# Kernel optimization log

Hardware: AMD Instinct MI355X
Metric: run time of the kernel (lower is better)

Reference implementation:

```python
import jax, jax.numpy as jnp
import numpy as np
import math

B, T, M, C, H = 4, 1024, 256, 512, 8
HD = C // H
NEG = -1e30


def setup_inputs() -> dict:
    key = jax.random.key(0)
    ks = jax.random.split(key, 16)
    s = 1.0 / math.sqrt(C)
    inp = {
        'x': jax.random.normal(ks[0], (B, T, C), jnp.float32),
        'y': jax.random.normal(ks[1], (B, M, C), jnp.float32),
        'attn_x_mask': jnp.tril(jnp.ones((T, T), bool))[None, None],  # causal (1,1,T,T)
        'Wqkv_x': jax.random.normal(ks[2], (C, 3 * C), jnp.float32) * s,
        'bqkv_x': jnp.zeros((3 * C,), jnp.float32),
        'Wqkv_y': jax.random.normal(ks[3], (C, 3 * C), jnp.float32) * s,
        'bqkv_y': jnp.zeros((3 * C,), jnp.float32),
        'w4x': jax.random.normal(ks[4], (H, HD), jnp.float32) * math.sqrt(1.0 / C / 3),
        'w4y': jax.random.normal(ks[5], (H, HD), jnp.float32) * math.sqrt(1.0 / C / 3),
        'w4xy': jax.random.normal(ks[6], (H, HD), jnp.float32) * math.sqrt(1.0 / C / 3),
        'Wgs': jax.random.normal(ks[7], (C, C), jnp.float32) * s,
        'bgs': jnp.zeros((C,), jnp.float32),
        'Wgc': jax.random.normal(ks[8], (C, C), jnp.float32) * s,
        'bgc': jnp.zeros((C,), jnp.float32),
        'Wp': jax.random.normal(ks[9], (C, C), jnp.float32) * s,
        'bp': jnp.zeros((C,), jnp.float32),
    }
    return inp


def _heads(t):
    b, n, c = t.shape
    return t.reshape(b, n, H, HD).transpose(0, 2, 1, 3)  # (B,H,N,HD)


def reference(x, y, attn_x_mask, Wqkv_x, bqkv_x, Wqkv_y, bqkv_y,
              w4x, w4y, w4xy, Wgs, bgs, Wgc, bgc, Wp, bp):
    q_x, k_x, v_x = [_heads(t) for t in jnp.split(x @ Wqkv_x + bqkv_x, 3, axis=-1)]
    q_y, k_y, v_y = [_heads(t) for t in jnp.split(y @ Wqkv_y + bqkv_y, 3, axis=-1)]
    scale = 1.0 / math.sqrt(HD)

    # additive bias attention: catt1 (per query-x), catt2 (per key-y), catt3 (bilinear)
    catt1 = jnp.einsum('bhtd,hd->bht', q_x, w4x)[..., :, None]          # (B,H,T,1)
    catt2 = jnp.einsum('bhmd,hd->bhm', q_y, w4y)[:, :, None, :]          # (B,H,1,M)
    catt3 = jnp.einsum('bhtd,bhmd->bhtm', q_x * w4xy[None, :, None, :], k_y) * scale
    catt = catt1 + catt2 + catt3                                         # (B,H,T,M)

    catt_x2y = jax.nn.softmax(catt, axis=-1)
    catt_y2x = jax.nn.softmax(catt, axis=-2)

    cval_x2y = jnp.einsum('bhtm,bhmd->bhtd', catt_x2y, v_y)
    cval_x2y = cval_x2y.transpose(0, 2, 1, 3).reshape(B, T, C)

    # product-of-attentions: (T,M) @ (M,T) -> (T,T)
    chain = jnp.einsum('bhtm,bhsm->bhts', catt_x2y, catt_y2x) * (1.0 / math.sqrt(M))
    chain = jnp.where(attn_x_mask, chain, NEG)
    chain = jax.nn.softmax(chain, axis=-1)
    cval_y2x = jnp.einsum('bhts,bhsd->bhtd', chain, v_x)
    cval_y2x = cval_y2x.transpose(0, 2, 1, 3).reshape(B, T, C)

    cval = cval_x2y + cval_y2x + x

    # masked self-attention
    satt = jnp.einsum('bhtd,bhsd->bhts', q_x, k_x) * scale
    satt = jnp.where(attn_x_mask, satt, NEG)
    satt = jax.nn.softmax(satt, axis=-1)
    sval = jnp.einsum('bhts,bhsd->bhtd', satt, v_x).transpose(0, 2, 1, 3).reshape(B, T, C)

    sgate = jax.nn.sigmoid(sval @ Wgs + bgs)
    cgate = jax.nn.sigmoid(cval @ Wgc + bgc)
    out = (sgate * cval + cgate * sval) @ Wp + bp
    return out
```

## Files before the change

### kernel.cpp

```cpp
#include <hip/hip_runtime.h>
#include <hip/hip_bf16.h>

typedef __hip_bfloat16 bf16;
using f4 = __attribute__((ext_vector_type(4))) float;
using s8 = __attribute__((ext_vector_type(8))) short;
using s4 = __attribute__((ext_vector_type(4))) short;

__device__ __forceinline__ void storeOut(float* p, float v) { *p = v; }
__device__ __forceinline__ void storeOut(bf16* p, float v) { *p = __float2bfloat16(v); }
__device__ __forceinline__ short bfs(float x) { return __builtin_bit_cast(short, __float2bfloat16(x)); }

constexpr int B_ = 4, T_ = 1024, M_ = 256, C_ = 512, H_ = 8, HD_ = 64, C3_ = 1536;

#define MFMA16(a, b, c) __builtin_amdgcn_mfma_f32_16x16x32_bf16((a), (b), (c), 0, 0, 0)

__global__ __launch_bounds__(256) void prep_kernel(
    const float* __restrict__ Wqkv_x, const float* __restrict__ Wqkv_y,
    const float* __restrict__ Wgs, const float* __restrict__ Wgc, const float* __restrict__ Wp,
    const float* __restrict__ x, const float* __restrict__ y,
    bf16* __restrict__ WT_x, bf16* __restrict__ WT_y, bf16* __restrict__ WT_gs,
    bf16* __restrict__ WT_gc, bf16* __restrict__ WT_p,
    bf16* __restrict__ x_bf, bf16* __restrict__ y_bf)
{
    __shared__ float Ls[64][65];
    const int tid = threadIdx.x;
    const int bid = blockIdx.x;
    if (bid < 576) {
        const float* W; bf16* WT; int N, t;
        if (bid < 192)      { W = Wqkv_x; WT = WT_x;  N = C3_; t = bid; }
        else if (bid < 384) { W = Wqkv_y; WT = WT_y;  N = C3_; t = bid - 192; }
        else if (bid < 448) { W = Wgs;    WT = WT_gs; N = C_;  t = bid - 384; }
        else if (bid < 512) { W = Wgc;    WT = WT_gc; N = C_;  t = bid - 448; }
        else                { W = Wp;     WT = WT_p;  N = C_;  t = bid - 512; }
        const int K = C_;
        const int tw = N >> 6;
        const int n0 = (t % tw) * 64, k0 = (t / tw) * 64;
        for (int i = tid; i < 1024; i += 256) {
            int kr = i >> 4, ng = i & 15;
            float4 v = *(const float4*)&W[(size_t)(k0 + kr) * N + n0 + ng * 4];
            Ls[ng * 4 + 0][kr] = v.x; Ls[ng * 4 + 1][kr] = v.y;
            Ls[ng * 4 + 2][kr] = v.z; Ls[ng * 4 + 3][kr] = v.w;
        }
        __syncthreads();
        for (int i = tid; i < 512; i += 256) {
            int n = i >> 3, kg = i & 7;
            s8 r;
            #pragma unroll
            for (int j = 0; j < 8; ++j) r[j] = bfs(Ls[n][kg * 8 + j]);
            *(s8*)&WT[(size_t)(n0 + n) * K + k0 + kg * 8] = r;
        }
    } else if (bid < 1600) {
        int i = (bid - 576) * 2048 + tid * 8;
        s8 r;
        #pragma unroll
        for (int j = 0; j < 8; ++j) r[j] = bfs(x[i + j]);
        *(s8*)&x_bf[i] = r;
    } else {
        int i = (bid - 1600) * 2048 + tid * 8;
        s8 r;
        #pragma unroll
        for (int j = 0; j < 8; ++j) r[j] = bfs(y[i + j]);
        *(s8*)&y_bf[i] = r;
    }
}

__global__ __launch_bounds__(256) void qwcatt_kernel(
    const bf16* __restrict__ qkv_x, const bf16* __restrict__ qkv_y,
    const float* __restrict__ w4x, const float* __restrict__ w4y,
    const float* __restrict__ w4xy,
    float* __restrict__ catt1b, float* __restrict__ catt2b, bf16* __restrict__ qw)
{
    const int bid = blockIdx.x;
    const int tid = threadIdx.x;
    if (bid < 160) {
        int i = bid * 256 + tid;
        const bf16* row; const float* w; float* out; int oi;
        if (i < 32768) {
            int bh = i >> 10, t = i & 1023, b = bh >> 3, h = bh & 7;
            row = qkv_x + (size_t)(b * T_ + t) * C3_ + h * HD_;
            w = w4x + h * HD_; out = catt1b; oi = i;
        } else {
            int j = i - 32768;
            int bh = j >> 8, m = j & 255, b = bh >> 3, h = bh & 7;
            row = qkv_y + (size_t)(b * M_ + m) * C3_ + h * HD_;
            w = w4y + h * HD_; out = catt2b; oi = j;
        }
        float s = 0.f;
        #pragma unroll
        for (int d = 0; d < HD_; ++d) s = fmaf(__bfloat162float(row[d]), w[d], s);
        out[oi] = s;
    } else {
        int o = ((bid - 160) * 256 + tid) * 8;
        int row = o >> 9, c = o & 511;
        const bf16* src = qkv_x + (size_t)row * C3_ + c;
        s8 r;
        #pragma unroll
        for (int j = 0; j < 8; ++j) r[j] = bfs(__bfloat162float(src[j]) * w4xy[c + j]);
        *(s8*)&qw[o] = r;
    }
}

template <typename OT>
__global__ __launch_bounds__(256) void gemm_staged_kernel(
    const bf16* __restrict__ A, const bf16* __restrict__ WT, const float* __restrict__ bias,
    OT* __restrict__ Cmat, int N, int K)
{
    __shared__ short Asb[128][72];
    __shared__ short Bsb[64][72];
    const int tid = threadIdx.x;
    const int wave = tid >> 6, lane = tid & 63;
    const int quad = lane >> 4, l16 = lane & 15;
    const int n0 = blockIdx.y * 64, m0 = blockIdx.x * 128;
    f4 acc[2][4];
    #pragma unroll
    for (int mt = 0; mt < 2; ++mt)
        #pragma unroll
        for (int nt = 0; nt < 4; ++nt) acc[mt][nt] = (f4)0.f;

    for (int k0 = 0; k0 < K; k0 += 64) {
        #pragma unroll
        for (int tl = 0; tl < 4; ++tl) {
            int g = tid + tl * 256, row = g >> 3, grp = g & 7;
            *(s8*)&Asb[row][grp * 8] = *(const s8*)&A[(size_t)(m0 + row) * K + k0 + grp * 8];
        }
        #pragma unroll
        for (int tl = 0; tl < 2; ++tl) {
            int g = tid + tl * 256, n = g >> 3, grp = g & 7;
            *(s8*)&Bsb[n][grp * 8] = *(const s8*)&WT[(size_t)(n0 + n) * K + k0 + grp * 8];
        }
        __syncthreads();
        #pragma unroll
        for (int ks = 0; ks < 2; ++ks) {
            s8 a0 = *(const s8*)&Asb[wave * 32 + l16][ks * 32 + quad * 8];
            s8 a1 = *(const s8*)&Asb[wave * 32 + 16 + l16][ks * 32 + quad * 8];
            #pragma unroll
            for (int nt = 0; nt < 4; ++nt) {
                s8 bv = *(const s8*)&Bsb[nt * 16 + l16][ks * 32 + quad * 8];
                acc[0][nt] = MFMA16(a0, bv, acc[0][nt]);
                acc[1][nt] = MFMA16(a1, bv, acc[1][nt]);
            }
        }
        __syncthreads();
    }
    #pragma unroll
    for (int mt = 0; mt < 2; ++mt)
        #pragma unroll
        for (int nt = 0; nt < 4; ++nt) {
            int col = n0 + nt * 16 + l16;
            float bb = bias[col];
            #pragma unroll
            for (int reg = 0; reg < 4; ++reg) {
                int row = m0 + wave * 32 + mt * 16 + quad * 4 + reg;
                storeOut(&Cmat[(size_t)row * N + col], acc[mt][nt][reg] + bb);
            }
        }
}

__global__ __launch_bounds__(256) void catt3r_kernel(
    const bf16* __restrict__ qw, const bf16* __restrict__ qkv_y,
    const float* __restrict__ catt1, const float* __restrict__ catt2,
    bf16* __restrict__ x2y, float* __restrict__ rowsum_, float* __restrict__ psum)
{
    __shared__ float redc[4][256];
    const int tid = threadIdx.x;
    const int wave = tid >> 6, lane = tid & 63;
    const int quad = lane >> 4, l16 = lane & 15;
    const int bh = blockIdx.x, b = bh >> 3, h = bh & 7;
    const int t0 = blockIdx.y * 64;
    f4 sc[4][4];
    #pragma unroll
    for (int mt = 0; mt < 4; ++mt)
        #pragma unroll
        for (int nt = 0; nt < 4; ++nt) sc[mt][nt] = (f4)0.f;

    const bf16* ap = qw + (size_t)(b * T_ + t0 + wave * 16 + l16) * C_ + h * HD_ + quad * 8;
    s8 a0 = *(const s8*)ap;
    s8 a1 = *(const s8*)(ap + 32);
    const bf16* bp = qkv_y + (size_t)(b * M_ + l16) * C3_ + C_ + h * HD_ + quad * 8;
    #pragma unroll
    for (int mt = 0; mt < 4; ++mt)
        #pragma unroll
        for (int nt = 0; nt < 4; ++nt) {
            const bf16* bq = bp + (size_t)(mt * 64 + nt * 16) * C3_;
            sc[mt][nt] = MFMA16(a0, *(const s8*)bq, sc[mt][nt]);
            sc[mt][nt] = MFMA16(a1, *(const s8*)(bq + 32), sc[mt][nt]);
        }

    float c1[4];
    #pragma unroll
    for (int reg = 0; reg < 4; ++reg)
        c1[reg] = catt1[bh * T_ + t0 + wave * 16 + quad * 4 + reg];
    #pragma unroll
    for (int mt = 0; mt < 4; ++mt)
        #pragma unroll
        for (int nt = 0; nt < 4; ++nt) {
            float c2 = catt2[bh * M_ + mt * 64 + nt * 16 + l16];
            #pragma unroll
            for (int reg = 0; reg < 4; ++reg)
                sc[mt][nt][reg] = __expf(sc[mt][nt][reg] * 0.125f + c1[reg] + c2);
        }

    #pragma unroll
    for (int reg = 0; reg < 4; ++reg) {
        float rs = 0.f;
        #pragma unroll
        for (int mt = 0; mt < 4; ++mt)
            #pragma unroll
            for (int nt = 0; nt < 4; ++nt) rs += sc[mt][nt][reg];
        rs += __shfl_xor(rs, 1); rs += __shfl_xor(rs, 2);
        rs += __shfl_xor(rs, 4); rs += __shfl_xor(rs, 8);
        const int t = t0 + wave * 16 + quad * 4 + reg;
        if (l16 == 0) rowsum_[bh * T_ + t] = rs;
        const float ri = 1.f / rs;
        #pragma unroll
        for (int mt = 0; mt < 4; ++mt)
            #pragma unroll
            for (int nt = 0; nt < 4; ++nt)
                x2y[((size_t)bh * T_ + t) * M_ + mt * 64 + nt * 16 + l16] =
                    __float2bfloat16(sc[mt][nt][reg] * ri);
    }

    #pragma unroll
    for (int mt = 0; mt < 4; ++mt)
        #pragma unroll
        for (int nt = 0; nt < 4; ++nt) {
            float es = sc[mt][nt][0] + sc[mt][nt][1] + sc[mt][nt][2] + sc[mt][nt][3];
            es += __shfl_xor(es, 16);
            es += __shfl_xor(es, 32);
            if (quad == 0) redc[wave][mt * 64 + nt * 16 + l16] = es;
        }
    __syncthreads();
    psum[((size_t)bh * 16 + blockIdx.y) * M_ + tid] =
        redc[0][tid] + redc[1][tid] + redc[2][tid] + redc[3][tid];
}

__global__ __launch_bounds__(256) void colfin_vtrans_kernel(
    const float* __restrict__ psum, float* __restrict__ colinv,
    const bf16* __restrict__ qkv_x, const bf16* __restrict__ qkv_y,
    bf16* __restrict__ vTx, bf16* __restrict__ vTy)
{
    __shared__ short Ls[64][68];
    const int tid = threadIdx.x;
    int bid = blockIdx.x;
    if (bid < 32) {
        const int bh = bid, m = tid;
        float s = 0.f;
        #pragma unroll
        for (int ch = 0; ch < 16; ++ch) s += psum[(bh * 16 + ch) * M_ + m];
        colinv[bh * M_ + m] = 1.f / s;
        return;
    }
    bid -= 32;
    const bf16* qkv; bf16* vT; int Nrows, bh, t0;
    if (bid < 512) { qkv = qkv_x; vT = vTx; Nrows = T_; bh = bid >> 4; t0 = (bid & 15) * 64; }
    else { bid -= 512; qkv = qkv_y; vT = vTy; Nrows = M_; bh = bid >> 2; t0 = (bid & 3) * 64; }
    const int b = bh >> 3, h = bh & 7;
    for (int i = tid; i < 4096; i += 256) {
        int tl = i >> 6, d = i & 63;
        Ls[d][tl] = __builtin_bit_cast(short,
            qkv[(size_t)(b * Nrows + t0 + tl) * C3_ + 2 * C_ + h * HD_ + d]);
    }
    __syncthreads();
    for (int i = tid; i < 4096; i += 256) {
        int d = i >> 6, tl = i & 63;
        vT[((size_t)bh * 64 + d) * Nrows + t0 + tl] = __builtin_bit_cast(bf16, Ls[d][tl]);
    }
}

__global__ __launch_bounds__(256) void y2xw_kernel(
    const bf16* __restrict__ x2y, const float* __restrict__ rowsum_,
    const float* __restrict__ colinv, bf16* __restrict__ y2x)
{
    const int i = (blockIdx.x * 256 + threadIdx.x) * 8;
    const int row = i >> 8, m = i & 255, bh = row >> 10;
    const float rs = rowsum_[row];
    s8 v = *(const s8*)&x2y[i];
    const float4 c0 = *(const float4*)&colinv[bh * M_ + m];
    const float4 c4 = *(const float4*)&colinv[bh * M_ + m + 4];
    float ci[8] = {c0.x, c0.y, c0.z, c0.w, c4.x, c4.y, c4.z, c4.w};
    s8 r;
    #pragma unroll
    for (int j = 0; j < 8; ++j)
        r[j] = bfs(__bfloat162float(__builtin_bit_cast(bf16, v[j])) * rs * ci[j]);
    *(s8*)&y2x[i] = r;
}

__global__ __launch_bounds__(256) void flash10_kernel(
    const bf16* __restrict__ x2y, const bf16* __restrict__ y2x,
    const bf16* __restrict__ vTx, const bf16* __restrict__ vTy,
    const bf16* __restrict__ qkv_x, const float* __restrict__ x,
    bf16* __restrict__ cval_bf, bf16* __restrict__ sval_bf)
{
    __shared__ short Kc[64][264];
    __shared__ short Ksf[64][72];
    __shared__ short Vb[64][72];
    __shared__ short Ps[4][16][68];
    const int tid = threadIdx.x;
    const int wave = tid >> 6, lane = tid & 63;
    const int quad = lane >> 4, l16 = lane & 15;
    const int bh = blockIdx.x, b = bh >> 3, h = bh & 7;
    const int jt = (blockIdx.y < 8) ? (15 - (int)blockIdx.y) : ((int)blockIdx.y - 8);
    const int rb = jt * 64 + wave * 16;
    const int nst = jt + 1;

    s8 qc[8], qs[2];
    {
        const bf16* qp = x2y + (size_t)(bh * T_ + rb + l16) * M_ + quad * 8;
        #pragma unroll
        for (int f = 0; f < 8; ++f) qc[f] = *(const s8*)(qp + f * 32);
        const bf16* qsp = qkv_x + (size_t)(b * T_ + rb + l16) * C3_ + h * HD_ + quad * 8;
        qs[0] = *(const s8*)qsp;
        qs[1] = *(const s8*)(qsp + 32);
    }

    f4 ocv[4];
    #pragma unroll
    for (int dt = 0; dt < 4; ++dt) ocv[dt] = (f4)0.f;
    {
        const bf16* vb = vTy + (size_t)(bh * 64 + l16) * M_ + quad * 8;
        #pragma unroll
        for (int f = 0; f < 8; ++f)
            #pragma unroll
            for (int dt = 0; dt < 4; ++dt) {
                s8 bv = *(const s8*)(vb + (size_t)dt * 16 * M_ + f * 32);
                ocv[dt] = MFMA16(qc[f], bv, ocv[dt]);
            }
    }

    f4 oc[4], os_[4];
    float lc[4] = {0.f, 0.f, 0.f, 0.f}, ls_[4] = {0.f, 0.f, 0.f, 0.f};
    #pragma unroll
    for (int dt = 0; dt < 4; ++dt) { oc[dt] = (f4)0.f; os_[dt] = (f4)0.f; }

    #pragma unroll
    for (int tl = 0; tl < 8; ++tl) {
        int g = tid + tl * 256, row = g >> 5, grp = g & 31;
        *(s8*)&Kc[row][grp * 8] = *(const s8*)&y2x[(size_t)(bh * T_ + row) * M_ + grp * 8];
    }
    #pragma unroll
    for (int tl = 0; tl < 2; ++tl) {
        int g = tid + tl * 256, row = g >> 3, grp = g & 7;
        *(s8*)&Ksf[row][grp * 8] =
            *(const s8*)&qkv_x[(size_t)(b * T_ + row) * C3_ + C_ + h * HD_ + grp * 8];
        *(s8*)&Vb[row][grp * 8] = *(const s8*)&vTx[(size_t)(bh * 64 + row) * T_ + grp * 8];
    }
    __syncthreads();

    for (int st = 0; st < nst; ++st) {
        const int s0 = st * 64;
        const bool pf = (st + 1) < nst;
        s8 kcp[8], ksp[2], vp[2];
        if (pf) {
            const int sn = s0 + 64;
            #pragma unroll
            for (int tl = 0; tl < 8; ++tl) {
                int g = tid + tl * 256, row = g >> 5, grp = g & 31;
                kcp[tl] = *(const s8*)&y2x[(size_t)(bh * T_ + sn + row) * M_ + grp * 8];
            }
            #pragma unroll
            for (int tl = 0; tl < 2; ++tl) {
                int g = tid + tl * 256, row = g >> 3, grp = g & 7;
                ksp[tl] = *(const s8*)&qkv_x[(size_t)(b * T_ + sn + row) * C3_ + C_ + h * HD_ + grp * 8];
                vp[tl] = *(const s8*)&vTx[(size_t)(bh * 64 + row) * T_ + sn + grp * 8];
            }
        }
        {
            f4 sc[4];
            #pragma unroll
            for (int nt = 0; nt < 4; ++nt) sc[nt] = (f4)0.f;
            #pragma unroll
            for (int f = 0; f < 8; ++f)
                #pragma unroll
                for (int nt = 0; nt < 4; ++nt) {
                    s8 bv = *(const s8*)&Kc[nt * 16 + l16][f * 32 + quad * 8];
                    sc[nt] = MFMA16(qc[f], bv, sc[nt]);
                }
            f4 ss[4];
            #pragma unroll
            for (int nt = 0; nt < 4; ++nt) ss[nt] = (f4)0.f;
            #pragma unroll
            for (int f = 0; f < 2; ++f)
                #pragma unroll
                for (int nt = 0; nt < 4; ++nt) {
                    s8 bv = *(const s8*)&Ksf[nt * 16 + l16][f * 32 + quad * 8];
                    ss[nt] = MFMA16(qs[f], bv, ss[nt]);
                }
            #pragma unroll
            for (int reg = 0; reg < 4; ++reg) {
                const int t_g = rb + quad * 4 + reg;
                #pragma unroll
                for (int nt = 0; nt < 4; ++nt) {
                    float pv = (s0 + nt * 16 + l16 <= t_g) ? __expf(sc[nt][reg] * (1.f / 16.f)) : 0.f;
                    lc[reg] += pv;
                    Ps[wave][quad * 4 + reg][nt * 16 + l16] = bfs(pv);
                }
            }
            #pragma unroll
            for (int ks = 0; ks < 2; ++ks) {
                const short* pp = &Ps[wave][l16][ks * 32 + quad * 8];
                s4 alo = *(const s4*)pp;
                s4 ahi = *(const s4*)(pp + 4);
                s8 a;
                a[0] = alo[0]; a[1] = alo[1]; a[2] = alo[2]; a[3] = alo[3];
                a[4] = ahi[0]; a[5] = ahi[1]; a[6] = ahi[2]; a[7] = ahi[3];
                #pragma unroll
                for (int dt = 0; dt < 4; ++dt) {
                    s8 bv = *(const s8*)&Vb[dt * 16 + l16][ks * 32 + quad * 8];
                    oc[dt] = MFMA16(a, bv, oc[dt]);
                }
            }
            #pragma unroll
            for (int reg = 0; reg < 4; ++reg) {
                const int t_g = rb + quad * 4 + reg;
                #pragma unroll
                for (int nt = 0; nt < 4; ++nt) {
                    float pv = (s0 + nt * 16 + l16 <= t_g) ? __expf(ss[nt][reg] * 0.125f) : 0.f;
                    ls_[reg] += pv;
                    Ps[wave][quad * 4 + reg][nt * 16 + l16] = bfs(pv);
                }
            }
            #pragma unroll
            for (int ks = 0; ks < 2; ++ks) {
                const short* pp = &Ps[wave][l16][ks * 32 + quad * 8];
                s4 alo = *(const s4*)pp;
                s4 ahi = *(const s4*)(pp + 4);
                s8 a;
                a[0] = alo[0]; a[1] = alo[1]; a[2] = alo[2]; a[3] = alo[3];
                a[4] = ahi[0]; a[5] = ahi[1]; a[6] = ahi[2]; a[7] = ahi[3];
                #pragma unroll
                for (int dt = 0; dt < 4; ++dt) {
                    s8 bv = *(const s8*)&Vb[dt * 16 + l16][ks * 32 + quad * 8];
                    os_[dt] = MFMA16(a, bv, os_[dt]);
                }
            }
        }
        __syncthreads();
        if (pf) {
            #pragma unroll
            for (int tl = 0; tl < 8; ++tl) {
                int g = tid + tl * 256, row = g >> 5, grp = g & 31;
                *(s8*)&Kc[row][grp * 8] = kcp[tl];
            }
            #pragma unroll
            for (int tl = 0; tl < 2; ++tl) {
                int g = tid + tl * 256, row = g >> 3, grp = g & 7;
                *(s8*)&Ksf[row][grp * 8] = ksp[tl];
                *(s8*)&Vb[row][grp * 8] = vp[tl];
            }
        }
        __syncthreads();
    }

    #pragma unroll
    for (int reg = 0; reg < 4; ++reg) {
        float l1 = lc[reg], l2 = ls_[reg];
        l1 += __shfl_xor(l1, 1); l1 += __shfl_xor(l1, 2);
        l1 += __shfl_xor(l1, 4); l1 += __shfl_xor(l1, 8);
        l2 += __shfl_xor(l2, 1); l2 += __shfl_xor(l2, 2);
        l2 += __shfl_xor(l2, 4); l2 += __shfl_xor(l2, 8);
        const float i1 = 1.f / l1, i2 = 1.f / l2;
        const int t = rb + quad * 4 + reg;
        #pragma unroll
        for (int dt = 0; dt < 4; ++dt) {
            size_t idx = (size_t)(b * T_ + t) * C_ + h * HD_ + dt * 16 + l16;
            float cv = ocv[dt][reg] + oc[dt][reg] * i1 + x[idx];
            cval_bf[idx] = __float2bfloat16(cv);
            float sv = os_[dt][reg] * i2;
            sval_bf[idx] = __float2bfloat16(sv);
        }
    }
}

__global__ __launch_bounds__(256) void gatefuse_kernel(
    const bf16* __restrict__ svalb, const bf16* __restrict__ cvalb,
    const bf16* __restrict__ WTgs, const bf16* __restrict__ WTgc,
    const float* __restrict__ bgs, const float* __restrict__ bgc,
    bf16* __restrict__ gated)
{
    __shared__ short Sb[128][72], Cb[128][72], W1b[64][72], W2b[64][72];
    const int tid = threadIdx.x;
    const int wave = tid >> 6, lane = tid & 63;
    const int quad = lane >> 4, l16 = lane & 15;
    const int n0 = blockIdx.y * 64, m0 = blockIdx.x * 128;
    f4 aS[2][4], aC[2][4];
    #pragma unroll
    for (int mt = 0; mt < 2; ++mt)
        #pragma unroll
        for (int nt = 0; nt < 4; ++nt) { aS[mt][nt] = (f4)0.f; aC[mt][nt] = (f4)0.f; }

    for (int k0 = 0; k0 < C_; k0 += 64) {
        #pragma unroll
        for (int tl = 0; tl < 4; ++tl) {
            int g = tid + tl * 256, row = g >> 3, grp = g & 7;
            *(s8*)&Sb[row][grp * 8] = *(const s8*)&svalb[(size_t)(m0 + row) * C_ + k0 + grp * 8];
            *(s8*)&Cb[row][grp * 8] = *(const s8*)&cvalb[(size_t)(m0 + row) * C_ + k0 + grp * 8];
        }
        #pragma unroll
        for (int tl = 0; tl < 2; ++tl) {
            int g = tid + tl * 256, n = g >> 3, grp = g & 7;
            *(s8*)&W1b[n][grp * 8] = *(const s8*)&WTgs[(size_t)(n0 + n) * C_ + k0 + grp * 8];
            *(s8*)&W2b[n][grp * 8] = *(const s8*)&WTgc[(size_t)(n0 + n) * C_ + k0 + grp * 8];
        }
        __syncthreads();
        #pragma unroll
        for (int ks = 0; ks < 2; ++ks) {
            s8 s0f = *(const s8*)&Sb[wave * 32 + l16][ks * 32 + quad * 8];
            s8 s1f = *(const s8*)&Sb[wave * 32 + 16 + l16][ks * 32 + quad * 8];
            s8 c0f = *(const s8*)&Cb[wave * 32 + l16][ks * 32 + quad * 8];
            s8 c1f = *(const s8*)&Cb[wave * 32 + 16 + l16][ks * 32 + quad * 8];
            #pragma unroll
            for (int nt = 0; nt < 4; ++nt) {
                s8 w1 = *(const s8*)&W1b[nt * 16 + l16][ks * 32 + quad * 8];
                s8 w2 = *(const s8*)&W2b[nt * 16 + l16][ks * 32 + quad * 8];
                aS[0][nt] = MFMA16(s0f, w1, aS[0][nt]);
                aS[1][nt] = MFMA16(s1f, w1, aS[1][nt]);
                aC[0][nt] = MFMA16(c0f, w2, aC[0][nt]);
                aC[1][nt] = MFMA16(c1f, w2, aC[1][nt]);
            }
        }
        __syncthreads();
    }
    #pragma unroll
    for (int mt = 0; mt < 2; ++mt)
        #pragma unroll
        for (int nt = 0; nt < 4; ++nt) {
            int col = n0 + nt * 16 + l16;
            float b1 = bgs[col], b2 = bgc[col];
            #pragma unroll
            for (int reg = 0; reg < 4; ++reg) {
                int row = m0 + wave * 32 + mt * 16 + quad * 4 + reg;
                size_t idx = (size_t)row * C_ + col;
                float gs = 1.f / (1.f + __expf(-(aS[mt][nt][reg] + b1)));
                float gc = 1.f / (1.f + __expf(-(aC[mt][nt][reg] + b2)));
                float cvv = __bfloat162float(cvalb[idx]);
                float svv = __bfloat162float(svalb[idx]);
                gated[idx] = __float2bfloat16(gs * cvv + gc * svv);
            }
        }
}

extern "C" void kernel_launch(void* const* d_in, const int* in_sizes, int n_in,
                              void* d_out, int out_size, void* d_ws, size_t ws_size,
                              hipStream_t stream)
{
    const float* x      = (const float*)d_in[0];
    const float* y      = (const float*)d_in[1];
    const float* Wqkv_x = (const float*)d_in[3];
    const float* bqkv_x = (const float*)d_in[4];
    const float* Wqkv_y = (const float*)d_in[5];
    const float* bqkv_y = (const float*)d_in[6];
    const float* w4x    = (const float*)d_in[7];
    const float* w4y    = (const float*)d_in[8];
    const float* w4xy   = (const float*)d_in[9];
    const float* Wgs    = (const float*)d_in[10];
    const float* bgs    = (const float*)d_in[11];
    const float* Wgc    = (const float*)d_in[12];
    const float* bgc    = (const float*)d_in[13];
    const float* Wp     = (const float*)d_in[14];
    const float* bp     = (const float*)d_in[15];

    float* ws = (float*)d_ws;
    bf16*  qkv_x_bf = (bf16*)(ws + 0);
    bf16*  qkv_y_bf = (bf16*)(ws + 3145728);
    bf16*  gated_bf = (bf16*)(ws + 3932160);
    bf16*  cval_bf  = (bf16*)(ws + 5242880);
    bf16*  x2y_bf   = (bf16*)(ws + 12320768);
    bf16*  x_bf     = x2y_bf;
    bf16*  y_bf     = (bf16*)(ws + 13369344);
    bf16*  y2x_bf   = (bf16*)(ws + 16515072);
    bf16*  vTx_bf   = (bf16*)(ws + 20709376);
    bf16*  vTy_bf   = (bf16*)(ws + 21757952);
    float* psum_    = ws + 22020096;
    bf16*  qw_bf    = (bf16*)(ws + 26214400);
    bf16*  sval_bf  = qw_bf;
    bf16*  WT_x     = (bf16*)(ws + 27262976);
    bf16*  WT_y     = (bf16*)(ws + 27656192);
    bf16*  WT_gs    = (bf16*)(ws + 28049408);
    bf16*  WT_gc    = (bf16*)(ws + 28180480);
    bf16*  WT_p    = (bf16*)(ws + 28311552);
    float* catt1b   = ws + 28442624;
    float* catt2b   = ws + 28475392;
    float* colinv   = ws + 28483584;
    float* rowsum_  = ws + 28491776;

    prep_kernel<<<1856, 256, 0, stream>>>(
        Wqkv_x, Wqkv_y, Wgs, Wgc, Wp, x, y,
        WT_x, WT_y, WT_gs, WT_gc, WT_p, x_bf, y_bf);

    gemm_staged_kernel<bf16><<<dim3(32, 24), 256, 0, stream>>>(x_bf, WT_x, bqkv_x, qkv_x_bf, C3_, C_);
    gemm_staged_kernel<bf16><<<dim3(8, 24), 256, 0, stream>>>(y_bf, WT_y, bqkv_y, qkv_y_bf, C3_, C_);

    qwcatt_kernel<<<1184, 256, 0, stream>>>(
        qkv_x_bf, qkv_y_bf, w4x, w4y, w4xy, catt1b, catt2b, qw_bf);

    catt3r_kernel<<<dim3(32, 16), 256, 0, stream>>>(
        qw_bf, qkv_y_bf, catt1b, catt2b, x2y_bf, rowsum_, psum_);

    colfin_vtrans_kernel<<<672, 256, 0, stream>>>(psum_, colinv, qkv_x_bf, qkv_y_bf, vTx_bf, vTy_bf);

    y2xw_kernel<<<4096, 256, 0, stream>>>(x2y_bf, rowsum_, colinv, y2x_bf);

    flash10_kernel<<<dim3(32, 16), 256, 0, stream>>>(
        x2y_bf, y2x_bf, vTx_bf, vTy_bf, qkv_x_bf, x, cval_bf, sval_bf);

    gatefuse_kernel<<<dim3(32, 8), 256, 0, stream>>>(
        sval_bf, cval_bf, WT_gs, WT_gc, bgs, bgc, gated_bf);

    gemm_staged_kernel<float><<<dim3(32, 8), 256, 0, stream>>>(
        gated_bf, WT_p, bp, (float*)d_out, C_, C_);
}
```

Baseline: 240.6 us.

## Pair short and long causal tiles per block with split-key wave groups

Replaces the flash attention kernel with a 512-thread version. Each block pairs a short causal query tile with its mirror long tile so every block runs nine balanced phases. One group of four waves handles the short tile fully and then the first part of the long tile. The other group handles the rest of the long tile, and the partial accumulators and row sums are merged through shared memory at the end. This removes the uneven per-block causal workload and tail imbalance, at the cost of doubled shared memory, an extra reduction and more synchronisation per phase.

Result: faster. 229.1 us (-4.8%).

```diff
diff --git a/kernel.cpp b/kernel.cpp
--- a/kernel.cpp
+++ b/kernel.cpp
@@ -285,30 +285,117 @@
     *(s8*)&y2x[i] = r;
 }
 
-__global__ __launch_bounds__(256) void flash10_kernel(
+__device__ __forceinline__ void attn_unit(
+    const short* __restrict__ Kc, const short* __restrict__ Ksf, const short* __restrict__ Vb,
+    short* __restrict__ PsW, const s8 qc[8], const s8 qs[2],
+    f4 (&oc)[4], f4 (&os)[4], float (&lc)[4], float (&ls)[4],
+    int s0, bool diag, int trow, int quad, int l16)
+{
+    f4 sc[4];
+    #pragma unroll
+    for (int nt = 0; nt < 4; ++nt) sc[nt] = (f4)0.f;
+    #pragma unroll
+    for (int f = 0; f < 8; ++f)
+        #pragma unroll
+        for (int nt = 0; nt < 4; ++nt) {
+            s8 bv = *(const s8*)&Kc[(nt * 16 + l16) * 264 + f * 32 + quad * 8];
+            sc[nt] = MFMA16(qc[f], bv, sc[nt]);
+        }
+    f4 ss[4];
+    #pragma unroll
+    for (int nt = 0; nt < 4; ++nt) ss[nt] = (f4)0.f;
+    #pragma unroll
+    for (int f = 0; f < 2; ++f)
+        #pragma unroll
+        for (int nt = 0; nt < 4; ++nt) {
+            s8 bv = *(const s8*)&Ksf[(nt * 16 + l16) * 72 + f * 32 + quad * 8];
+            ss[nt] = MFMA16(qs[f], bv, ss[nt]);
+        }
+    #pragma unroll
+    for (int reg = 0; reg < 4; ++reg) {
+        const int t_g = trow + quad * 4 + reg;
+        #pragma unroll
+        for (int nt = 0; nt < 4; ++nt) {
+            float pv = __expf(sc[nt][reg] * 0.0625f);
+            if (diag && (s0 + nt * 16 + l16 > t_g)) pv = 0.f;
+            lc[reg] += pv;
+            PsW[(quad * 4 + reg) * 68 + nt * 16 + l16] = bfs(pv);
+        }
+    }
+    #pragma unroll
+    for (int ks = 0; ks < 2; ++ks) {
+        const short* pp = &PsW[l16 * 68 + ks * 32 + quad * 8];
+        s4 alo = *(const s4*)pp;
+        s4 ahi = *(const s4*)(pp + 4);
+        s8 a;
+        a[0] = alo[0]; a[1] = alo[1]; a[2] = alo[2]; a[3] = alo[3];
+        a[4] = ahi[0]; a[5] = ahi[1]; a[6] = ahi[2]; a[7] = ahi[3];
+        #pragma unroll
+        for (int dt = 0; dt < 4; ++dt) {
+            s8 bv = *(const s8*)&Vb[(dt * 16 + l16) * 72 + ks * 32 + quad * 8];
+            oc[dt] = MFMA16(a, bv, oc[dt]);
+        }
+    }
+    #pragma unroll
+    for (int reg = 0; reg < 4; ++reg) {
+        const int t_g = trow + quad * 4 + reg;
+        #pragma unroll
+        for (int nt = 0; nt < 4; ++nt) {
+            float pv = __expf(ss[nt][reg] * 0.125f);
+            if (diag && (s0 + nt * 16 + l16 > t_g)) pv = 0.f;
+            ls[reg] += pv;
+            PsW[(quad * 4 + reg) * 68 + nt * 16 + l16] = bfs(pv);
+        }
+    }
+    #pragma unroll
+    for (int ks = 0; ks < 2; ++ks) {
+        const short* pp = &PsW[l16 * 68 + ks * 32 + quad * 8];
+        s4 alo = *(const s4*)pp;
+        s4 ahi = *(const s4*)(pp + 4);
+        s8 a;
+        a[0] = alo[0]; a[1] = alo[1]; a[2] = alo[2]; a[3] = alo[3];
+        a[4] = ahi[0]; a[5] = ahi[1]; a[6] = ahi[2]; a[7] = ahi[3];
+        #pragma unroll
+        for (int dt = 0; dt < 4; ++dt) {
+            s8 bv = *(const s8*)&Vb[(dt * 16 + l16) * 72 + ks * 32 + quad * 8];
+            os[dt] = MFMA16(a, bv, os[dt]);
+        }
+    }
+}
+
+__global__ __launch_bounds__(512, 2) void flash11_kernel(
     const bf16* __restrict__ x2y, const bf16* __restrict__ y2x,
     const bf16* __restrict__ vTx, const bf16* __restrict__ vTy,
     const bf16* __restrict__ qkv_x, const float* __restrict__ x,
     bf16* __restrict__ cval_bf, bf16* __restrict__ sval_bf)
 {
-    __shared__ short Kc[64][264];
-    __shared__ short Ksf[64][72];
-    __shared__ short Vb[64][72];
-    __shared__ short Ps[4][16][68];
+    __shared__ short KcA[64][264], KcB[64][264];
+    __shared__ short KsfA[64][72], KsfB[64][72];
+    __shared__ short VbA[64][72], VbB[64][72];
+    __shared__ short Ps[8][16][68];
     const int tid = threadIdx.x;
     const int wave = tid >> 6, lane = tid & 63;
     const int quad = lane >> 4, l16 = lane & 15;
     const int bh = blockIdx.x, b = bh >> 3, h = bh & 7;
-    const int jt = (blockIdx.y < 8) ? (15 - (int)blockIdx.y) : ((int)blockIdx.y - 8);
-    const int rb = jt * 64 + wave * 16;
-    const int nst = jt + 1;
+    const int p = blockIdx.y;
+    const int w = wave & 3;
+    const bool gA = wave < 4;
+    const int q2t = 15 - p;
+    const int rb1 = p * 64 + w * 16, rb2 = q2t * 64 + w * 16;
+    short* PsW = &Ps[wave][0][0];
+    const int tidg = tid & 255;
+
+    short (*Kc)[264] = gA ? KcA : KcB;
+    short (*Ksf)[72] = gA ? KsfA : KsfB;
+    short (*Vv)[72]  = gA ? VbA : VbB;
 
     s8 qc[8], qs[2];
     {
-        const bf16* qp = x2y + (size_t)(bh * T_ + rb + l16) * M_ + quad * 8;
+        const int rq = gA ? rb1 : rb2;
+        const bf16* qp = x2y + (size_t)(bh * T_ + rq + l16) * M_ + quad * 8;
         #pragma unroll
         for (int f = 0; f < 8; ++f) qc[f] = *(const s8*)(qp + f * 32);
-        const bf16* qsp = qkv_x + (size_t)(b * T_ + rb + l16) * C3_ + h * HD_ + quad * 8;
+        const bf16* qsp = qkv_x + (size_t)(b * T_ + rq + l16) * C3_ + h * HD_ + quad * 8;
         qs[0] = *(const s8*)qsp;
         qs[1] = *(const s8*)(qsp + 32);
     }
@@ -332,141 +419,151 @@
     #pragma unroll
     for (int dt = 0; dt < 4; ++dt) { oc[dt] = (f4)0.f; os_[dt] = (f4)0.f; }
 
-    #pragma unroll
-    for (int tl = 0; tl < 8; ++tl) {
-        int g = tid + tl * 256, row = g >> 5, grp = g & 31;
-        *(s8*)&Kc[row][grp * 8] = *(const s8*)&y2x[(size_t)(bh * T_ + row) * M_ + grp * 8];
-    }
-    #pragma unroll
-    for (int tl = 0; tl < 2; ++tl) {
-        int g = tid + tl * 256, row = g >> 3, grp = g & 7;
-        *(s8*)&Ksf[row][grp * 8] =
-            *(const s8*)&qkv_x[(size_t)(b * T_ + row) * C3_ + C_ + h * HD_ + grp * 8];
-        *(s8*)&Vb[row][grp * 8] = *(const s8*)&vTx[(size_t)(bh * 64 + row) * T_ + grp * 8];
+    {
+        const int s = gA ? 0 : (8 - p);
+        #pragma unroll
+        for (int tl = 0; tl < 8; ++tl) {
+            int g = tidg + tl * 256, row = g >> 5, grp = g & 31;
+            *(s8*)&Kc[row][grp * 8] = *(const s8*)&y2x[(size_t)(bh * T_ + s * 64 + row) * M_ + grp * 8];
+        }
+        #pragma unroll
+        for (int tl = 0; tl < 2; ++tl) {
+            int g = tidg + tl * 256, row = g >> 3, grp = g & 7;
+            *(s8*)&Ksf[row][grp * 8] =
+                *(const s8*)&qkv_x[(size_t)(b * T_ + s * 64 + row) * C3_ + C_ + h * HD_ + grp * 8];
+            *(s8*)&Vv[row][grp * 8] = *(const s8*)&vTx[(size_t)(bh * 64 + row) * T_ + s * 64 + grp * 8];
+        }
     }
     __syncthreads();
 
-    for (int st = 0; st < nst; ++st) {
-        const int s0 = st * 64;
-        const bool pf = (st + 1) < nst;
-        s8 kcp[8], ksp[2], vp[2];
-        if (pf) {
-            const int sn = s0 + 64;
+    for (int ph = 0; ph < 9; ++ph) {
+        int s, trow; bool active, diag;
+        if (gA) {
+            if (ph <= p) { s = ph;         diag = (ph == p); trow = rb1; }
+            else         { s = ph - p - 1; diag = false;     trow = rb2; }
+            active = true;
+        } else {
+            s = 8 - p + ph; diag = (ph == 7); trow = rb2;
+            active = (ph < 8);
+        }
+        int sn;
+        if (gA) sn = (ph < p) ? (ph + 1) : ((ph == p) ? 0 : ((ph < 8) ? (ph - p) : -1));
+        else    sn = (ph < 7) ? (s + 1) : -1;
+
+        s8 kc[8], ks[2], vb[2];
+        if (sn >= 0) {
             #pragma unroll
             for (int tl = 0; tl < 8; ++tl) {
-                int g = tid + tl * 256, row = g >> 5, grp = g & 31;
-                kcp[tl] = *(const s8*)&y2x[(size_t)(bh * T_ + sn + row) * M_ + grp * 8];
+                int g = tidg + tl * 256, row = g >> 5, grp = g & 31;
+                kc[tl] = *(const s8*)&y2x[(size_t)(bh * T_ + sn * 64 + row) * M_ + grp * 8];
             }
             #pragma unroll
             for (int tl = 0; tl < 2; ++tl) {
-                int g = tid + tl * 256, row = g >> 3, grp = g & 7;
-                ksp[tl] = *(const s8*)&qkv_x[(size_t)(b * T_ + sn + row) * C3_ + C_ + h * HD_ + grp * 8];
-                vp[tl] = *(const s8*)&vTx[(size_t)(bh * 64 + row) * T_ + sn + grp * 8];
-            }
-        }
-        {
-            f4 sc[4];
-            #pragma unroll
-            for (int nt = 0; nt < 4; ++nt) sc[nt] = (f4)0.f;
-            #pragma unroll
-            for (int f = 0; f < 8; ++f)
-                #pragma unroll
-                for (int nt = 0; nt < 4; ++nt) {
-                    s8 bv = *(const s8*)&Kc[nt * 16 + l16][f * 32 + quad * 8];
-                    sc[nt] = MFMA16(qc[f], bv, sc[nt]);
-                }
-            f4 ss[4];
-            #pragma unroll
-            for (int nt = 0; nt < 4; ++nt) ss[nt] = (f4)0.f;
-            #pragma unroll
-            for (int f = 0; f < 2; ++f)
-                #pragma unroll
-                for (int nt = 0; nt < 4; ++nt) {
-                    s8 bv = *(const s8*)&Ksf[nt * 16 + l16][f * 32 + quad * 8];
-                    ss[nt] = MFMA16(qs[f], bv, ss[nt]);
-                }
+                int g = tidg + tl * 256, row = g >> 3, grp = g & 7;
+                ks[tl] = *(const s8*)&qkv_x[(size_t)(b * T_ + sn * 64 + row) * C3_ + C_ + h * HD_ + grp * 8];
+                vb[tl] = *(const s8*)&vTx[(size_t)(bh * 64 + row) * T_ + sn * 64 + grp * 8];
+            }
+        }
+
+        if (active)
+            attn_unit(&Kc[0][0], &Ksf[0][0], &Vv[0][0], PsW, qc, qs,
+                      oc, os_, lc, ls_, s * 64, diag, trow, quad, l16);
+
+        if (gA && ph == p) {
             #pragma unroll
             for (int reg = 0; reg < 4; ++reg) {
-                const int t_g = rb + quad * 4 + reg;
-                #pragma unroll
-                for (int nt = 0; nt < 4; ++nt) {
-                    float pv = (s0 + nt * 16 + l16 <= t_g) ? __expf(sc[nt][reg] * (1.f / 16.f)) : 0.f;
-                    lc[reg] += pv;
-                    Ps[wave][quad * 4 + reg][nt * 16 + l16] = bfs(pv);
-                }
-            }
-            #pragma unroll
-            for (int ks = 0; ks < 2; ++ks) {
-                const short* pp = &Ps[wave][l16][ks * 32 + quad * 8];
-                s4 alo = *(const s4*)pp;
-                s4 ahi = *(const s4*)(pp + 4);
-                s8 a;
-                a[0] = alo[0]; a[1] = alo[1]; a[2] = alo[2]; a[3] = alo[3];
-                a[4] = ahi[0]; a[5] = ahi[1]; a[6] = ahi[2]; a[7] = ahi[3];
+                float l1 = lc[reg], l2 = ls_[reg];
+                l1 += __shfl_xor(l1, 1); l1 += __shfl_xor(l1, 2);
+                l1 += __shfl_xor(l1, 4); l1 += __shfl_xor(l1, 8);
+                l2 += __shfl_xor(l2, 1); l2 += __shfl_xor(l2, 2);
+                l2 += __shfl_xor(l2, 4); l2 += __shfl_xor(l2, 8);
+                const float i1 = 1.f / l1, i2 = 1.f / l2;
+                const int t = rb1 + quad * 4 + reg;
                 #pragma unroll
                 for (int dt = 0; dt < 4; ++dt) {
-                    s8 bv = *(const s8*)&Vb[dt * 16 + l16][ks * 32 + quad * 8];
-                    oc[dt] = MFMA16(a, bv, oc[dt]);
+                    size_t idx = (size_t)(b * T_ + t) * C_ + h * HD_ + dt * 16 + l16;
+                    cval_bf[idx] = __float2bfloat16(ocv[dt][reg] + oc[dt][reg] * i1 + x[idx]);
+                    sval_bf[idx] = __float2bfloat16(os_[dt][reg] * i2);
                 }
             }
+            const bf16* qp = x2y + (size_t)(bh * T_ + rb2 + l16) * M_ + quad * 8;
+            #pragma unroll
+            for (int f = 0; f < 8; ++f) qc[f] = *(const s8*)(qp + f * 32);
+            const bf16* qsp = qkv_x + (size_t)(b * T_ + rb2 + l16) * C3_ + h * HD_ + quad * 8;
+            qs[0] = *(const s8*)qsp;
+            qs[1] = *(const s8*)(qsp + 32);
+            #pragma unroll
+            for (int dt = 0; dt < 4; ++dt) { oc[dt] = (f4)0.f; os_[dt] = (f4)0.f; }
+            #pragma unroll
+            for (int reg = 0; reg < 4; ++reg) { lc[reg] = 0.f; ls_[reg] = 0.f; }
+        }
+
+        __syncthreads();
+        if (sn >= 0) {
+            #pragma unroll
+            for (int tl = 0; tl < 8; ++tl) {
+                int g = tidg + tl * 256, row = g >> 5, grp = g & 31;
+                *(s8*)&Kc[row][grp * 8] = kc[tl];
+            }
+            #pragma unroll
+            for (int tl = 0; tl < 2; ++tl) {
+                int g = tidg + tl * 256, row = g >> 3, grp = g & 7;
+                *(s8*)&Ksf[row][grp * 8] = ks[tl];
+                *(s8*)&Vv[row][grp * 8] = vb[tl];
+            }
+        }
+        __syncthreads();
+    }
+
+    if (gA) {
+        float* fb = (float*)&KcA[0][0];
+        float* lb = (float*)&KsfA[0][0];
+        const int base = w * 64 + lane;
+        #pragma unroll
+        for (int dt = 0; dt < 4; ++dt)
             #pragma unroll
             for (int reg = 0; reg < 4; ++reg) {
-                const int t_g = rb + quad * 4 + reg;
-                #pragma unroll
-                for (int nt = 0; nt < 4; ++nt) {
-                    float pv = (s0 + nt * 16 + l16 <= t_g) ? __expf(ss[nt][reg] * 0.125f) : 0.f;
-                    ls_[reg] += pv;
-                    Ps[wave][quad * 4 + reg][nt * 16 + l16] = bfs(pv);
-                }
-            }
-            #pragma unroll
-            for (int ks = 0; ks < 2; ++ks) {
-                const short* pp = &Ps[wave][l16][ks * 32 + quad * 8];
-                s4 alo = *(const s4*)pp;
-                s4 ahi = *(const s4*)(pp + 4);
-                s8 a;
-                a[0] = alo[0]; a[1] = alo[1]; a[2] = alo[2]; a[3] = alo[3];
-                a[4] = ahi[0]; a[5] = ahi[1]; a[6] = ahi[2]; a[7] = ahi[3];
-                #pragma unroll
-                for (int dt = 0; dt < 4; ++dt) {
-                    s8 bv = *(const s8*)&Vb[dt * 16 + l16][ks * 32 + quad * 8];
-                    os_[dt] = MFMA16(a, bv, os_[dt]);
-                }
-            }
-        }
-        __syncthreads();
-        if (pf) {
-            #pragma unroll
-            for (int tl = 0; tl < 8; ++tl) {
-                int g = tid + tl * 256, row = g >> 5, grp = g & 31;
-                *(s8*)&Kc[row][grp * 8] = kcp[tl];
-            }
-            #pragma unroll
-            for (int tl = 0; tl < 2; ++tl) {
-                int g = tid + tl * 256, row = g >> 3, grp = g & 7;
-                *(s8*)&Ksf[row][grp * 8] = ksp[tl];
-                *(s8*)&Vb[row][grp * 8] = vp[tl];
-            }
-        }
-        __syncthreads();
-    }
-
-    #pragma unroll
-    for (int reg = 0; reg < 4; ++reg) {
-        float l1 = lc[reg], l2 = ls_[reg];
-        l1 += __shfl_xor(l1, 1); l1 += __shfl_xor(l1, 2);
-        l1 += __shfl_xor(l1, 4); l1 += __shfl_xor(l1, 8);
-        l2 += __shfl_xor(l2, 1); l2 += __shfl_xor(l2, 2);
-        l2 += __shfl_xor(l2, 4); l2 += __shfl_xor(l2, 8);
-        const float i1 = 1.f / l1, i2 = 1.f / l2;
-        const int t = rb + quad * 4 + reg;
-        #pragma unroll
-        for (int dt = 0; dt < 4; ++dt) {
-            size_t idx = (size_t)(b * T_ + t) * C_ + h * HD_ + dt * 16 + l16;
-            float cv = ocv[dt][reg] + oc[dt][reg] * i1 + x[idx];
-            cval_bf[idx] = __float2bfloat16(cv);
-            float sv = os_[dt][reg] * i2;
-            sval_bf[idx] = __float2bfloat16(sv);
+                fb[base * 33 + dt * 4 + reg] = oc[dt][reg];
+                fb[base * 33 + 16 + dt * 4 + reg] = os_[dt][reg];
+            }
+        #pragma unroll
+        for (int reg = 0; reg < 4; ++reg) {
+            lb[base * 9 + reg] = lc[reg];
+            lb[base * 9 + 4 + reg] = ls_[reg];
+        }
+    }
+    __syncthreads();
+    if (!gA) {
+        const float* fb = (const float*)&KcA[0][0];
+        const float* lb = (const float*)&KsfA[0][0];
+        const int base = w * 64 + lane;
+        #pragma unroll
+        for (int dt = 0; dt < 4; ++dt)
+            #pragma unroll
+            for (int reg = 0; reg < 4; ++reg) {
+                oc[dt][reg] += fb[base * 33 + dt * 4 + reg];
+                os_[dt][reg] += fb[base * 33 + 16 + dt * 4 + reg];
+            }
+        #pragma unroll
+        for (int reg = 0; reg < 4; ++reg) {
+            lc[reg] += lb[base * 9 + reg];
+            ls_[reg] += lb[base * 9 + 4 + reg];
+        }
+        #pragma unroll
+        for (int reg = 0; reg < 4; ++reg) {
+            float l1 = lc[reg], l2 = ls_[reg];
+            l1 += __shfl_xor(l1, 1); l1 += __shfl_xor(l1, 2);
+            l1 += __shfl_xor(l1, 4); l1 += __shfl_xor(l1, 8);
+            l2 += __shfl_xor(l2, 1); l2 += __shfl_xor(l2, 2);
+            l2 += __shfl_xor(l2, 4); l2 += __shfl_xor(l2, 8);
+            const float i1 = 1.f / l1, i2 = 1.f / l2;
+            const int t = rb2 + quad * 4 + reg;
+            #pragma unroll
+            for (int dt = 0; dt < 4; ++dt) {
+                size_t idx = (size_t)(b * T_ + t) * C_ + h * HD_ + dt * 16 + l16;
+                cval_bf[idx] = __float2bfloat16(ocv[dt][reg] + oc[dt][reg] * i1 + x[idx]);
+                sval_bf[idx] = __float2bfloat16(os_[dt][reg] * i2);
+            }
         }
     }
 }
@@ -600,7 +697,7 @@
 
     y2xw_kernel<<<4096, 256, 0, stream>>>(x2y_bf, rowsum_, colinv, y2x_bf);
 
-    flash10_kernel<<<dim3(32, 16), 256, 0, stream>>>(
+    flash11_kernel<<<dim3(32, 8), 512, 0, stream>>>(
         x2y_bf, y2x_bf, vTx_bf, vTy_bf, qkv_x_bf, x, cval_bf, sval_bf);
 
     gatefuse_kernel<<<dim3(32, 8), 256, 0, stream>>>(
```
